# Optimization experiments

Hardware: AMD Instinct MI355X
Metric: run time of the kernel (lower is better)

## Reference

```python
import jax, jax.numpy as jnp
import numpy as np

B, S, E, H = 2, 2048, 768, 12
D = E // H  # head_dim = 64
EPS = 1e-5


def layernorm(x, g, b):
    mu = jnp.mean(x, axis=-1, keepdims=True)
    var = jnp.mean(jnp.square(x - mu), axis=-1, keepdims=True)
    return (x - mu) * jax.lax.rsqrt(var + EPS) * g + b


def setup_inputs() -> dict:
    key = jax.random.key(0)
    ks = jax.random.split(key, 8)
    std = 0.02
    return {
        "x": jax.random.normal(ks[0], (B, S, E), dtype=jnp.float32),
        "ln1_g": jnp.ones((E,), jnp.float32),
        "ln1_b": jnp.zeros((E,), jnp.float32),
        "w_attn": jax.random.normal(ks[1], (E, 3 * E), jnp.float32) * std,
        "b_attn": jnp.zeros((3 * E,), jnp.float32),
        "w_aproj": jax.random.normal(ks[2], (E, E), jnp.float32) * std,
        "b_aproj": jnp.zeros((E,), jnp.float32),
        "ln2_g": jnp.ones((E,), jnp.float32),
        "ln2_b": jnp.zeros((E,), jnp.float32),
        "w_fc": jax.random.normal(ks[3], (E, 4 * E), jnp.float32) * std,
        "b_fc": jnp.zeros((4 * E,), jnp.float32),
        "w_fproj": jax.random.normal(ks[4], (4 * E, E), jnp.float32) * std,
        "b_fproj": jnp.zeros((E,), jnp.float32),
    }


def reference(x, ln1_g, ln1_b, w_attn, b_attn, w_aproj, b_aproj,
              ln2_g, ln2_b, w_fc, b_fc, w_fproj, b_fproj):
    # --- attention sub-block (pre-LN) ---
    residual = x
    h = layernorm(x, ln1_g, ln1_b)
    qkv = h @ w_attn + b_attn                      # [B,S,3E]
    q, k, v = jnp.split(qkv, 3, axis=-1)
    # split heads -> [B,H,S,D]
    q = q.reshape(B, S, H, D).transpose(0, 2, 1, 3)
    k = k.reshape(B, S, H, D).transpose(0, 2, 1, 3)
    v = v.reshape(B, S, H, D).transpose(0, 2, 1, 3)
    # NOTE: original module applies NO 1/sqrt(D) scaling
    scores = jnp.einsum('bhqd,bhkd->bhqk', q, k)   # [B,H,S,S]
    causal = jnp.tril(jnp.ones((S, S), dtype=bool))
    mask_val = jnp.finfo(scores.dtype).min
    scores = jnp.where(causal, scores, mask_val)
    attn = jax.nn.softmax(scores, axis=-1)          # dropout = identity (eval)
    out = jnp.einsum('bhqk,bhkd->bhqd', attn, v)   # [B,H,S,D]
    out = out.transpose(0, 2, 1, 3).reshape(B, S, E)
    out = out @ w_aproj + b_aproj
    x = residual + out
    # --- MLP sub-block (pre-LN) ---
    residual = x
    h = layernorm(x, ln2_g, ln2_b)
    h = h @ w_fc + b_fc
    h = jax.nn.gelu(h, approximate=False)          # nn.GELU() exact erf form
    h = h @ w_fproj + b_fproj
    return residual + h
```

## Files before the change

### kernel.cpp

```cpp
#include <hip/hip_runtime.h>
#include <math.h>

#define B_ 2
#define S_ 2048
#define E_ 768
#define H_ 12
#define D_ 64
#define M_TOT (B_*S_)

typedef __attribute__((ext_vector_type(8))) short s16x8;
typedef __attribute__((ext_vector_type(4))) float f32x4;

__device__ __forceinline__ unsigned short f2bf(float f) {
  union { float f; unsigned u; } v; v.f = f;
  unsigned r = (v.u + 0x7fffu + ((v.u >> 16) & 1u)) >> 16;
  return (unsigned short)r;
}

__device__ __forceinline__ int swz(int r) { return ((r >> 3) ^ r) & 7; }

__device__ __forceinline__ void gload_lds16(const unsigned short* g, unsigned short* l) {
  __builtin_amdgcn_global_load_lds(
      (const __attribute__((address_space(1))) void*)g,
      (__attribute__((address_space(3))) void*)l, 16, 0, 0);
}

__global__ __launch_bounds__(256) void tconv_kernel(const float* __restrict__ in,
                                                    unsigned short* __restrict__ out,
                                                    int R, int C) {
  __shared__ float tile[32][33];
  int c0 = blockIdx.x * 32, r0 = blockIdx.y * 32;
  int t = threadIdx.x;
  int cl = t & 31, rl = t >> 5;
  #pragma unroll
  for (int p = 0; p < 4; ++p)
    tile[rl + p*8][cl] = in[(size_t)(r0 + rl + p*8)*C + c0 + cl];
  __syncthreads();
  int rl2 = t & 31, cl2 = t >> 5;
  #pragma unroll
  for (int p = 0; p < 4; ++p)
    out[(size_t)(c0 + cl2 + p*8)*R + r0 + rl2] = f2bf(tile[rl2][cl2 + p*8]);
}

__global__ __launch_bounds__(256) void vtrans_kernel(const unsigned short* __restrict__ qkv,
                                                     unsigned short* __restrict__ vt) {
  __shared__ unsigned short tile[32][33];
  int s0 = blockIdx.x * 32;
  int by = blockIdx.y;
  int bh = by >> 1, dh = by & 1;
  int b = bh / H_, h = bh % H_;
  int t = threadIdx.x;
  const unsigned short* src = qkv + (size_t)(b*S_)*2304 + 2*E_ + h*64 + dh*32;
  int srow = t >> 3, dq = t & 7;
  ushort4 v = *reinterpret_cast<const ushort4*>(src + (size_t)(s0 + srow)*2304 + dq*4);
  tile[srow][dq*4+0] = v.x; tile[srow][dq*4+1] = v.y;
  tile[srow][dq*4+2] = v.z; tile[srow][dq*4+3] = v.w;
  __syncthreads();
  int drow = t >> 3, sq = t & 7;
  ushort4 o;
  o.x = tile[sq*4+0][drow]; o.y = tile[sq*4+1][drow];
  o.z = tile[sq*4+2][drow]; o.w = tile[sq*4+3][drow];
  *reinterpret_cast<ushort4*>(vt + (size_t)(bh*64 + dh*32 + drow)*S_ + s0 + sq*4) = o;
}

__global__ __launch_bounds__(64) void ln_kernel(const float* __restrict__ x,
                                                const float* __restrict__ g,
                                                const float* __restrict__ b,
                                                unsigned short* __restrict__ out) {
  int row = blockIdx.x;
  int lane = threadIdx.x;
  const float* xr = x + (size_t)row * E_;
  float4 v[3];
  float s = 0.f, sq = 0.f;
  #pragma unroll
  for (int p = 0; p < 3; ++p) {
    v[p] = *reinterpret_cast<const float4*>(xr + p*256 + lane*4);
    s  += v[p].x + v[p].y + v[p].z + v[p].w;
    sq += v[p].x*v[p].x + v[p].y*v[p].y + v[p].z*v[p].z + v[p].w*v[p].w;
  }
  #pragma unroll
  for (int off = 32; off; off >>= 1) {
    s  += __shfl_xor(s,  off, 64);
    sq += __shfl_xor(sq, off, 64);
  }
  float mu  = s * (1.f/E_);
  float var = sq * (1.f/E_) - mu*mu;
  float rstd = rsqrtf(var + 1e-5f);
  unsigned short* orow = out + (size_t)row * E_;
  #pragma unroll
  for (int p = 0; p < 3; ++p) {
    int c = p*256 + lane*4;
    float4 gg = *reinterpret_cast<const float4*>(g + c);
    float4 bb = *reinterpret_cast<const float4*>(b + c);
    ushort4 o;
    o.x = f2bf((v[p].x-mu)*rstd*gg.x + bb.x);
    o.y = f2bf((v[p].y-mu)*rstd*gg.y + bb.y);
    o.z = f2bf((v[p].z-mu)*rstd*gg.z + bb.z);
    o.w = f2bf((v[p].w-mu)*rstd*gg.w + bb.w);
    *reinterpret_cast<ushort4*>(orow + c) = o;
  }
}

template<int MODE, int BM>
__global__ __launch_bounds__(256) void gemm_kernel(
    const unsigned short* __restrict__ A,
    const unsigned short* __restrict__ Wt,
    const float* __restrict__ bias,
    const float* __restrict__ res,
    unsigned short* __restrict__ outb,
    float* __restrict__ outf,
    int M, int N, int K)
{
  constexpr int Mi = BM / 32;
  __shared__ __align__(16) unsigned short As[2][BM*64];
  __shared__ __align__(16) unsigned short Ws[2][128*64];

  int nwg = gridDim.x, bid = blockIdx.x;
  int cpx = nwg >> 3;
  int sw = (bid & 7) * cpx + (bid >> 3);
  int nbm = M / BM;
  int m0 = (sw % nbm) * BM, n0 = (sw / nbm) * 128;

  int t = threadIdx.x, lane = t & 63, w = t >> 6;
  f32x4 acc[Mi][4] = {};
  int KT = K >> 6;

  auto stage = [&](int kt, int buf) {
    int k0 = kt << 6;
    #pragma unroll
    for (int p = 0; p < BM/32; ++p) {
      int off = p*2048 + w*512 + lane*8;
      int r = off >> 6;
      int slot = (off & 63) >> 3;
      int k8 = slot ^ swz(r);
      gload_lds16(A + (size_t)(m0 + r)*K + k0 + k8*8, &As[buf][p*2048 + w*512]);
    }
    #pragma unroll
    for (int p = 0; p < 4; ++p) {
      int off = p*2048 + w*512 + lane*8;
      int r = off >> 6;
      int slot = (off & 63) >> 3;
      int k8 = slot ^ swz(r);
      gload_lds16(Wt + (size_t)(n0 + r)*K + k0 + k8*8, &Ws[buf][p*2048 + w*512]);
    }
  };

  int wm = (w >> 1) * (BM/2), wn = (w & 1) * 64;
  int li = lane & 15, g = lane >> 4;

  stage(0, 0);
  __syncthreads();
  for (int kt = 0; kt < KT; ++kt) {
    int cur = kt & 1;
    if (kt + 1 < KT) stage(kt + 1, cur ^ 1);
    #pragma unroll
    for (int kk = 0; kk < 2; ++kk) {
      s16x8 af[Mi], bf[4];
      int k8 = kk*4 + g;
      #pragma unroll
      for (int mi = 0; mi < Mi; ++mi) {
        int r = wm + mi*16 + li;
        af[mi] = *reinterpret_cast<const s16x8*>(&As[cur][r*64 + ((k8 ^ swz(r)) << 3)]);
      }
      #pragma unroll
      for (int ni = 0; ni < 4; ++ni) {
        int r = wn + ni*16 + li;
        bf[ni] = *reinterpret_cast<const s16x8*>(&Ws[cur][r*64 + ((k8 ^ swz(r)) << 3)]);
      }
      #pragma unroll
      for (int mi = 0; mi < Mi; ++mi)
        #pragma unroll
        for (int ni = 0; ni < 4; ++ni)
          acc[mi][ni] = __builtin_amdgcn_mfma_f32_16x16x32_bf16(af[mi], bf[ni], acc[mi][ni], 0, 0, 0);
    }
    __syncthreads();
  }

  #pragma unroll
  for (int mi = 0; mi < Mi; ++mi) {
    #pragma unroll
    for (int j = 0; j < 4; ++j) {
      int row = m0 + wm + mi*16 + g*4 + j;
      #pragma unroll
      for (int ni = 0; ni < 4; ++ni) {
        int col = n0 + wn + ni*16 + li;
        float v = acc[mi][ni][j] + bias[col];
        size_t idx = (size_t)row * N + col;
        if (MODE == 0) {
          outb[idx] = f2bf(v);
        } else if (MODE == 1) {
          outf[idx] = v + res[idx];
        } else {
          float gv = 0.5f * v * (1.f + erff(v * 0.70710678118f));
          outb[idx] = f2bf(gv);
        }
      }
    }
  }
}

__global__ __launch_bounds__(256) void attn_kernel(const unsigned short* __restrict__ qkv,
                                                   const unsigned short* __restrict__ vtg,
                                                   unsigned short* __restrict__ out,
                                                   float* __restrict__ part) {
  __shared__ __align__(16) unsigned short Ks[2][64*64];
  __shared__ __align__(16) unsigned short Vs[2][64*64];
  __shared__ __align__(16) unsigned short Pl[4][16*64];

  int gid = blockIdx.x;
  int bh = gid / 80, zi = gid % 80;
  int qt, ch;
  if (zi < 8)       { qt = zi;                ch = 0; }
  else if (zi < 24) { qt = 8  + ((zi-8)>>1);  ch = (zi-8) & 1; }
  else if (zi < 48) { qt = 16 + (zi-24)/3;    ch = (zi-24) % 3; }
  else              { qt = 24 + ((zi-48)>>2); ch = (zi-48) & 3; }
  int nc = (qt + 8) >> 3;
  int b = bh / H_, h = bh % H_;
  int t = threadIdx.x, lane = t & 63, w = t >> 6;
  int li = lane & 15, g = lane >> 4;
  const size_t rs = 3*E_;
  const unsigned short* base  = qkv + (size_t)b * S_ * rs;
  const unsigned short* kbase = base + E_ + h*64;
  const unsigned short* vbase = vtg + (size_t)bh * 64 * S_;

  int q0w = qt*64 + w*16;
  int qmin = q0w;
  s16x8 qf[2];
  #pragma unroll
  for (int f = 0; f < 2; ++f)
    qf[f] = *reinterpret_cast<const s16x8*>(base + (size_t)(q0w + li)*rs + h*64 + f*32 + g*8);

  float mrun = -1e30f, lrun = 0.f;
  f32x4 o[4] = {};

  auto stage = [&](int kvt, int buf) {
    int kv0 = kvt * 64;
    #pragma unroll
    for (int p = 0; p < 2; ++p) {
      int off = p*2048 + w*512 + lane*8;
      int r = off >> 6;
      int slot = (off & 63) >> 3;
      gload_lds16(kbase + (size_t)(kv0 + r)*rs + ((slot ^ (r & 7)) << 3),
                  &Ks[buf][p*2048 + w*512]);
      gload_lds16(vbase + (size_t)r*S_ + kv0 + ((slot ^ (r & 7)) << 3),
                  &Vs[buf][p*2048 + w*512]);
    }
  };

  int t0 = (ch * 512) >> 6;
  int t1 = min((ch + 1) * 512, (qt + 1) * 64) >> 6;

  stage(t0, 0);
  __syncthreads();

  for (int kt = t0; kt < t1; ++kt) {
    int cur = (kt - t0) & 1;
    if (kt + 1 < t1) stage(kt + 1, cur ^ 1);
    int kv0 = kt * 64;

    if (kv0 <= qmin + 15) {
      f32x4 pm[4];
      #pragma unroll
      for (int nh = 0; nh < 4; ++nh) {
        int r = nh*16 + li;
        int sw = r & 7;
        s16x8 kf0 = *reinterpret_cast<const s16x8*>(&Ks[cur][r*64 + ((g       ^ sw) << 3)]);
        s16x8 kf1 = *reinterpret_cast<const s16x8*>(&Ks[cur][r*64 + (((4 + g) ^ sw) << 3)]);
        f32x4 z = {};
        z = __builtin_amdgcn_mfma_f32_16x16x32_bf16(kf0, qf[0], z, 0, 0, 0);
        z = __builtin_amdgcn_mfma_f32_16x16x32_bf16(kf1, qf[1], z, 0, 0, 0);
        pm[nh] = z;
      }

      if (kv0 + 63 > qmin) {
        int q = qmin + li;
        #pragma unroll
        for (int nh = 0; nh < 4; ++nh)
          #pragma unroll
          for (int j = 0; j < 4; ++j) {
            int k = kv0 + nh*16 + g*4 + j;
            pm[nh][j] = (k <= q) ? pm[nh][j] : -1e30f;
          }
      }

      float tm = -1e30f;
      #pragma unroll
      for (int nh = 0; nh < 4; ++nh)
        tm = fmaxf(tm, fmaxf(fmaxf(pm[nh][0], pm[nh][1]), fmaxf(pm[nh][2], pm[nh][3])));
      tm = fmaxf(tm, __shfl_xor(tm, 16, 64));
      tm = fmaxf(tm, __shfl_xor(tm, 32, 64));
      float mnew = fmaxf(mrun, tm);
      float sc = __expf(mrun - mnew);
      mrun = mnew;

      unsigned short* Pw = Pl[w];
      float ps = 0.f;
      #pragma unroll
      for (int nh = 0; nh < 4; ++nh) {
        #pragma unroll
        for (int j = 0; j < 4; ++j) { pm[nh][j] = __expf(pm[nh][j] - mnew); ps += pm[nh][j]; }
        uint2 pk;
        pk.x = (unsigned)f2bf(pm[nh][0]) | ((unsigned)f2bf(pm[nh][1]) << 16);
        pk.y = (unsigned)f2bf(pm[nh][2]) | ((unsigned)f2bf(pm[nh][3]) << 16);
        int slot = 2*nh + (g >> 1);
        *reinterpret_cast<uint2*>(Pw + li*64 + ((slot ^ (li & 7)) << 3) + (g & 1)*4) = pk;
      }
      ps += __shfl_xor(ps, 16, 64);
      ps += __shfl_xor(ps, 32, 64);
      lrun = lrun*sc + ps;

      float scr[4];
      #pragma unroll
      for (int j = 0; j < 4; ++j) scr[j] = __shfl(sc, g*4 + j, 64);
      #pragma unroll
      for (int nc2 = 0; nc2 < 4; ++nc2)
        #pragma unroll
        for (int j = 0; j < 4; ++j) o[nc2][j] *= scr[j];

      asm volatile("s_waitcnt lgkmcnt(0)" ::: "memory");
      __builtin_amdgcn_sched_barrier(0);

      #pragma unroll
      for (int kk = 0; kk < 2; ++kk) {
        s16x8 pf = *reinterpret_cast<const s16x8*>(Pw + li*64 + (((kk*4 + g) ^ (li & 7)) << 3));
        #pragma unroll
        for (int nc2 = 0; nc2 < 4; ++nc2) {
          int r = nc2*16 + li;
          s16x8 vf = *reinterpret_cast<const s16x8*>(&Vs[cur][r*64 + (((kk*4 + g) ^ (r & 7)) << 3)]);
          o[nc2] = __builtin_amdgcn_mfma_f32_16x16x32_bf16(pf, vf, o[nc2], 0, 0, 0);
        }
      }
    }
    __syncthreads();
  }

  if (nc == 1) {
    float linv = 1.f / lrun;
    float lj[4];
    #pragma unroll
    for (int j = 0; j < 4; ++j) lj[j] = __shfl(linv, g*4 + j, 64);
    #pragma unroll
    for (int nc2 = 0; nc2 < 4; ++nc2)
      #pragma unroll
      for (int j = 0; j < 4; ++j)
        out[(size_t)(b*S_ + q0w + g*4 + j)*E_ + h*64 + nc2*16 + li] = f2bf(o[nc2][j] * lj[j]);
  } else {
    int cumP = (qt < 16) ? (qt-8)*2 : (qt < 24) ? 16 + (qt-16)*3 : 40 + (qt-24)*4;
    float* ps_ = part + (size_t)(bh*72 + cumP + ch) * 4224;
    #pragma unroll
    for (int nc2 = 0; nc2 < 4; ++nc2)
      #pragma unroll
      for (int j = 0; j < 4; ++j)
        ps_[(w*16 + g*4 + j)*64 + nc2*16 + li] = o[nc2][j];
    if (g == 0) {
      ps_[4096 + w*16 + li] = mrun;
      ps_[4160 + w*16 + li] = lrun;
    }
  }
}

__global__ __launch_bounds__(256) void merge_kernel(const float* __restrict__ part,
                                                    unsigned short* __restrict__ out) {
  int qt = 8 + blockIdx.x;
  int bh = blockIdx.y;
  int b = bh / H_, h = bh % H_;
  int t = threadIdx.x;
  int r = t >> 2, dg = (t & 3) * 16;
  int nc = (qt + 8) >> 3;
  int cumP = (qt < 16) ? (qt-8)*2 : (qt < 24) ? 16 + (qt-16)*3 : 40 + (qt-24)*4;
  const float* base = part + (size_t)(bh*72 + cumP) * 4224;

  float mv[4], lv[4];
  float M = -1e30f;
  for (int c = 0; c < nc; ++c) {
    mv[c] = base[c*4224 + 4096 + r];
    lv[c] = base[c*4224 + 4160 + r];
    M = fmaxf(M, mv[c]);
  }
  float wv[4], L = 0.f;
  for (int c = 0; c < nc; ++c) {
    wv[c] = __expf(mv[c] - M);
    L += lv[c] * wv[c];
  }
  float inv = 1.f / L;
  float acc[16] = {};
  for (int c = 0; c < nc; ++c) {
    const float* oc = base + c*4224 + r*64 + dg;
    #pragma unroll
    for (int j = 0; j < 16; j += 4) {
      float4 v = *reinterpret_cast<const float4*>(oc + j);
      acc[j+0] += v.x * wv[c];
      acc[j+1] += v.y * wv[c];
      acc[j+2] += v.z * wv[c];
      acc[j+3] += v.w * wv[c];
    }
  }
  unsigned short* orow = out + (size_t)(b*S_ + qt*64 + r)*E_ + h*64 + dg;
  ushort4 o4;
  #pragma unroll
  for (int j = 0; j < 16; j += 4) {
    o4.x = f2bf(acc[j+0]*inv); o4.y = f2bf(acc[j+1]*inv);
    o4.z = f2bf(acc[j+2]*inv); o4.w = f2bf(acc[j+3]*inv);
    *reinterpret_cast<ushort4*>(orow + j) = o4;
  }
}

extern "C" void kernel_launch(void* const* d_in, const int* in_sizes, int n_in,
                              void* d_out, int out_size, void* d_ws, size_t ws_size,
                              hipStream_t stream) {
  const float* x       = (const float*)d_in[0];
  const float* ln1g    = (const float*)d_in[1];
  const float* ln1b    = (const float*)d_in[2];
  const float* w_attn  = (const float*)d_in[3];
  const float* b_attn  = (const float*)d_in[4];
  const float* w_aproj = (const float*)d_in[5];
  const float* b_aproj = (const float*)d_in[6];
  const float* ln2g    = (const float*)d_in[7];
  const float* ln2b    = (const float*)d_in[8];
  const float* w_fc    = (const float*)d_in[9];
  const float* b_fc    = (const float*)d_in[10];
  const float* w_fproj = (const float*)d_in[11];
  const float* b_fproj = (const float*)d_in[12];
  float* out = (float*)d_out;

  char* ws = (char*)d_ws;
  unsigned short* h1       = (unsigned short*)(ws + 0);
  unsigned short* qkv      = (unsigned short*)(ws + 6291456);
  unsigned short* attno    = (unsigned short*)(ws + 25165824);
  float*          x2       = (float*)(ws + 31457280);
  unsigned short* h2       = (unsigned short*)(ws + 44040192);
  unsigned short* h3       = (unsigned short*)(ws + 50331648);
  unsigned short* wt_attn  = (unsigned short*)(ws + 75497472);
  unsigned short* wt_aproj = (unsigned short*)(ws + 79036416);
  unsigned short* wt_fc    = (unsigned short*)(ws + 80216064);
  unsigned short* wt_fproj = (unsigned short*)(ws + 84934656);
  unsigned short* vtg      = (unsigned short*)(ws + 89653248);
  float*          apart    = (float*)(ws + 44040192);

  tconv_kernel<<<dim3(2304/32,  768/32), 256, 0, stream>>>(w_attn,  wt_attn,  768, 2304);
  tconv_kernel<<<dim3( 768/32,  768/32), 256, 0, stream>>>(w_aproj, wt_aproj, 768,  768);
  tconv_kernel<<<dim3(3072/32,  768/32), 256, 0, stream>>>(w_fc,    wt_fc,    768, 3072);
  tconv_kernel<<<dim3( 768/32, 3072/32), 256, 0, stream>>>(w_fproj, wt_fproj, 3072, 768);

  ln_kernel<<<dim3(M_TOT), dim3(64), 0, stream>>>(x, ln1g, ln1b, h1);
  gemm_kernel<0,128><<<dim3((2304/128)*(M_TOT/128)), 256, 0, stream>>>(h1, wt_attn, b_attn, nullptr, qkv, nullptr, M_TOT, 2304, 768);
  vtrans_kernel<<<dim3(S_/32, B_*H_*2), 256, 0, stream>>>(qkv, vtg);
  attn_kernel<<<dim3(24*80), dim3(256), 0, stream>>>(qkv, vtg, attno, apart);
  merge_kernel<<<dim3(24, 24), dim3(256), 0, stream>>>(apart, attno);
  gemm_kernel<1,64><<<dim3((768/128)*(M_TOT/64)), 256, 0, stream>>>(attno, wt_aproj, b_aproj, x, nullptr, x2, M_TOT, 768, 768);
  ln_kernel<<<dim3(M_TOT), dim3(64), 0, stream>>>(x2, ln2g, ln2b, h2);
  gemm_kernel<2,128><<<dim3((3072/128)*(M_TOT/128)), 256, 0, stream>>>(h2, wt_fc, b_fc, nullptr, h3, nullptr, M_TOT, 3072, 768);
  gemm_kernel<1,64><<<dim3((768/128)*(M_TOT/64)), 256, 0, stream>>>(h3, wt_fproj, b_fproj, x2, nullptr, out, M_TOT, 768, 3072);
}
```

Before: 212.7 us.

## Triple-buffer GEMM LDS stages with partial vmcnt waits for deeper prefetch

```diff
diff --git a/kernel.cpp b/kernel.cpp
--- a/kernel.cpp
+++ b/kernel.cpp
@@ -23,6 +23,16 @@
   __builtin_amdgcn_global_load_lds(
       (const __attribute__((address_space(1))) void*)g,
       (__attribute__((address_space(3))) void*)l, 16, 0, 0);
+}
+
+template<int N>
+__device__ __forceinline__ void wait_vm_barrier() {
+  __builtin_amdgcn_sched_barrier(0);
+  if constexpr (N == 8)      asm volatile("s_waitcnt vmcnt(8)" ::: "memory");
+  else if constexpr (N == 6) asm volatile("s_waitcnt vmcnt(6)" ::: "memory");
+  else                       asm volatile("s_waitcnt vmcnt(0)" ::: "memory");
+  __builtin_amdgcn_s_barrier();
+  __builtin_amdgcn_sched_barrier(0);
 }
 
 __global__ __launch_bounds__(256) void tconv_kernel(const float* __restrict__ in,
@@ -112,8 +122,9 @@
     int M, int N, int K)
 {
   constexpr int Mi = BM / 32;
-  __shared__ __align__(16) unsigned short As[2][BM*64];
-  __shared__ __align__(16) unsigned short Ws[2][128*64];
+  constexpr int LPW = BM/32 + 4;
+  __shared__ __align__(16) unsigned short As[3][BM*64];
+  __shared__ __align__(16) unsigned short Ws[3][128*64];
 
   int nwg = gridDim.x, bid = blockIdx.x;
   int cpx = nwg >> 3;
@@ -148,11 +159,7 @@
   int wm = (w >> 1) * (BM/2), wn = (w & 1) * 64;
   int li = lane & 15, g = lane >> 4;
 
-  stage(0, 0);
-  __syncthreads();
-  for (int kt = 0; kt < KT; ++kt) {
-    int cur = kt & 1;
-    if (kt + 1 < KT) stage(kt + 1, cur ^ 1);
+  auto compute = [&](int buf) {
     #pragma unroll
     for (int kk = 0; kk < 2; ++kk) {
       s16x8 af[Mi], bf[4];
@@ -160,12 +167,12 @@
       #pragma unroll
       for (int mi = 0; mi < Mi; ++mi) {
         int r = wm + mi*16 + li;
-        af[mi] = *reinterpret_cast<const s16x8*>(&As[cur][r*64 + ((k8 ^ swz(r)) << 3)]);
+        af[mi] = *reinterpret_cast<const s16x8*>(&As[buf][r*64 + ((k8 ^ swz(r)) << 3)]);
       }
       #pragma unroll
       for (int ni = 0; ni < 4; ++ni) {
         int r = wn + ni*16 + li;
-        bf[ni] = *reinterpret_cast<const s16x8*>(&Ws[cur][r*64 + ((k8 ^ swz(r)) << 3)]);
+        bf[ni] = *reinterpret_cast<const s16x8*>(&Ws[buf][r*64 + ((k8 ^ swz(r)) << 3)]);
       }
       #pragma unroll
       for (int mi = 0; mi < Mi; ++mi)
@@ -173,7 +180,23 @@
         for (int ni = 0; ni < 4; ++ni)
           acc[mi][ni] = __builtin_amdgcn_mfma_f32_16x16x32_bf16(af[mi], bf[ni], acc[mi][ni], 0, 0, 0);
     }
-    __syncthreads();
+  };
+
+  stage(0, 0);
+  stage(1, 1);
+  wait_vm_barrier<LPW>();
+
+  int cc = 0, sc = 2;
+  for (int kt = 0; kt < KT; ++kt) {
+    bool pre = (kt + 2 < KT);
+    if (pre) stage(kt + 2, sc);
+    compute(cc);
+    if (kt + 1 < KT) {
+      if (pre) wait_vm_barrier<LPW>();
+      else     wait_vm_barrier<0>();
+    }
+    cc = (cc == 2) ? 0 : cc + 1;
+    sc = (sc == 2) ? 0 : sc + 1;
   }
 
   #pragma unroll
```

Result: slower. 259.3 us (+21.9%).
